# Kernel optimization log

Measured on AMD Instinct MI355X. Metric: run time of the kernel, lower is better.

The kernel has to match this reference:

```python
import jax, jax.numpy as jnp
import numpy as np

B, H, L, DIM = 4, 8, 1024, 256
D = DIM // H  # per-head dim
DEPTH, LAYER_I = 12, 1  # layer_index < depth//4 -> adjacency masking active


def _gcn(xh, adj, W):
    # One graph-convolution layer (GCN used as q/k/v projection in the repo):
    # support = x @ W per head, then aggregate with the (attention-)adjacency.
    # xh: [b,h,t,d], adj: [b,h,l,t], W: [d,d] -> [b,h,l,d]
    return jnp.einsum('bhlt,bhtd->bhld', adj, xh @ W)


def _split_heads(x):
    # 'b t (h d) -> b h t d'
    b, t, _ = x.shape
    return x.reshape(b, t, H, D).transpose(0, 2, 1, 3)


def _merge_heads(v):
    # 'b h t d -> b t (h d)'
    b, h, t, d = v.shape
    return v.transpose(0, 2, 1, 3).reshape(b, t, h * d)


def setup_inputs() -> dict:
    key = jax.random.key(0)
    ks = jax.random.split(key, 9)
    x = jax.random.normal(ks[0], (B, L, DIM), jnp.float32)
    resize_x = jax.random.normal(ks[1], (B, L, DIM), jnpp := jnp.float32) if False else jax.random.normal(ks[1], (B, L, DIM), jnp.float32)
    eye = jnp.eye(L, dtype=jnp.float32)[None, None]  # self-loops so no all-masked rows
    adj = jnp.clip((jax.random.uniform(ks[2], (B, H, L, L)) < 0.1).astype(jnp.float32) + eye, 0.0, 1.0)
    adj_resize = jnp.clip((jax.random.uniform(ks[3], (B, H, L, L)) < 0.1).astype(jnp.float32) + eye, 0.0, 1.0)
    s = D ** -0.5
    Wq = jax.random.normal(ks[4], (D, D), jnp.float32) * s
    Wk = jax.random.normal(ks[5], (D, D), jnp.float32) * s
    Wv = jax.random.normal(ks[6], (D, D), jnp.float32) * s
    R = jax.random.normal(ks[7], (H, H), jnp.float32)  # 'randomatrix' head-mixing param
    Wp = jax.random.normal(ks[8], (DIM, DIM), jnp.float32) * (DIM ** -0.5)  # proj_v (no bias)
    return {'x': x, 'resize_x': resize_x, 'adj': adj, 'adj_resize': adj_resize,
            'Wq': Wq, 'Wk': Wk, 'Wv': Wv, 'R': R, 'Wp': Wp}


def reference(x, resize_x, adj, adj_resize, Wq, Wk, Wv, R, Wp):
    scale = DIM ** -0.5  # note: torch code scales by dim**-0.5 (full dim, not d_head)
    xh = _split_heads(x)          # [b,h,l,d]
    rxh = _split_heads(resize_x)  # [b,h,t,d]
    q = _gcn(xh, adj, Wq)         # [b,h,l,d]
    k = _gcn(rxh, adj_resize, Wk)  # [b,h,t,d]
    attn = jnp.einsum('bhld,bhtd->bhlt', q, k) * scale
    attn = jax.nn.leaky_relu(attn, negative_slope=0.01)
    # cross-head mixing with learned HxH matrix: out[b,i] = sum_h R[i,h]*attn[b,h]
    attn = jnp.einsum('ih,bhlt->bilt', R, attn)
    if LAYER_I < DEPTH // 4:
        attn = jnp.where(adj > 0, attn, -jnp.inf)
    A = jax.nn.softmax(attn, axis=-1)                      # rep_adj
    Ar = jax.nn.softmax(A.transpose(0, 1, 3, 2), axis=-1)  # dual softmax on transpose
    v = _merge_heads(_gcn(xh, A, Wv))
    out = jax.nn.gelu(v, approximate=False) @ Wp
    vr = _merge_heads(_gcn(rxh, Ar, Wv))
    out_resize = jax.nn.gelu(vr, approximate=False) @ Wp
    return out, out_resize, A, Ar
```

## Files before the change

### kernel.cpp

```cpp
#include <hip/hip_runtime.h>
#include <hip/hip_bf16.h>
#include <math.h>

#define BB 4
#define HH 8
#define LL 1024
#define DD 32
#define DIMM 256

typedef unsigned short u16;
typedef short bf16x8 __attribute__((ext_vector_type(8)));
typedef float f32x4 __attribute__((ext_vector_type(4)));

__device__ __forceinline__ float bu2f(u16 s) {
  union { unsigned int u; float f; } cv; cv.u = ((unsigned int)s) << 16; return cv.f;
}
__device__ __forceinline__ u16 f2bu(float f) {
  union { float f; unsigned int u; } cv; cv.f = f;
  unsigned int u = cv.u;
  u += 0x7FFFu + ((u >> 16) & 1u);
  return (u16)(u >> 16);
}
__device__ __forceinline__ short f2bs(float f) {
  return (short)__bfloat16_as_ushort(__float2bfloat16(f));
}

__global__ __launch_bounds__(256) void k_proj(
    const float* __restrict__ x, const float* __restrict__ rx,
    const float* __restrict__ Wq, const float* __restrict__ Wk, const float* __restrict__ Wv,
    u16* __restrict__ xqT_hi, u16* __restrict__ xqT_lo,
    u16* __restrict__ xkT_hi, u16* __restrict__ xkT_lo,
    u16* __restrict__ xvT_hi, u16* __restrict__ xvrT_hi) {
  __shared__ float wq[32][32], wk[32][32], wv[32][32];
  __shared__ float xs[8][32], rxs[8][32];
  __shared__ float tq_[32][9], tk_[32][9], tv_[32][9], tvr_[32][9];
  int tid = threadIdx.x, bid = blockIdx.x;
  int chunk = bid & 127, h = (bid >> 7) & 7, b = bid >> 10;
  int t0 = chunk << 3;
  for (int i = tid; i < 1024; i += 256) {
    int r = i >> 5, c = i & 31;
    wq[r][c] = Wq[i]; wk[r][c] = Wk[i]; wv[r][c] = Wv[i];
  }
  int d = tid & 31, tl = tid >> 5;
  size_t xoff = ((size_t)b * LL + t0 + tl) * DIMM + h * 32 + d;
  xs[tl][d]  = x[xoff];
  rxs[tl][d] = rx[xoff];
  __syncthreads();
  float aq = 0.f, ak = 0.f, av = 0.f, ar = 0.f;
#pragma unroll
  for (int dp = 0; dp < 32; ++dp) {
    float xv_ = xs[tl][dp], rv_ = rxs[tl][dp];
    aq += xv_ * wq[dp][d];
    ak += rv_ * wk[dp][d];
    av += xv_ * wv[dp][d];
    ar += rv_ * wv[dp][d];
  }
  tq_[d][tl] = aq; tk_[d][tl] = ak; tv_[d][tl] = av; tvr_[d][tl] = ar;
  __syncthreads();
  int d2 = tid >> 3, t2 = tid & 7;
  size_t obase = ((size_t)((b * HH + h) * DD + d2)) * LL + t0 + t2;
  {
    float v = tq_[d2][t2]; u16 hi = f2bu(v);
    xqT_hi[obase] = hi; xqT_lo[obase] = f2bu(v - bu2f(hi));
  }
  {
    float v = tk_[d2][t2]; u16 hi = f2bu(v);
    xkT_hi[obase] = hi; xkT_lo[obase] = f2bu(v - bu2f(hi));
  }
  xvT_hi[obase]  = f2bu(tv_[d2][t2]);
  xvrT_hi[obase] = f2bu(tvr_[d2][t2]);
}

template<int PREC, int OUT_SPLIT>
__global__ __launch_bounds__(256) void k_wmat2(
    const float* __restrict__ wA, const float* __restrict__ wB,
    const u16* __restrict__ sAh, const u16* __restrict__ sAl,
    const u16* __restrict__ sBh, const u16* __restrict__ sBl,
    float* __restrict__ dA, float* __restrict__ dB,
    u16* __restrict__ dAhi, u16* __restrict__ dAlo,
    u16* __restrict__ dBhi, u16* __restrict__ dBlo) {
  int tid = threadIdx.x, bid = blockIdx.x;
  int sel = bid >> 9;
  const float* w  = sel ? wB : wA;
  const u16* sh   = sel ? sBh : sAh;
  const u16* sl   = sel ? sBl : sAl;
  float* dst      = sel ? dB : dA;
  u16* dhi        = sel ? dBhi : dAhi;
  u16* dlo        = sel ? dBlo : dAlo;
  int b2 = bid & 511;
  int lc = b2 & 15, bh = b2 >> 4;
  int wave = tid >> 6, lane = tid & 63;
  int l0 = (lc << 6) + (wave << 4);
  int col = lane & 15, g = lane >> 4;
  const float* wrow = w + ((size_t)bh * LL + l0 + col) * LL + (g << 3);
  const u16* b0h = sh + ((size_t)bh * DD + col) * LL + (g << 3);
  const u16* b1h = b0h + 16 * LL;
  const u16* b0l = PREC == 2 ? sl + ((size_t)bh * DD + col) * LL + (g << 3) : nullptr;
  const u16* b1l = PREC == 2 ? b0l + 16 * LL : nullptr;
  f32x4 acc0 = {0.f, 0.f, 0.f, 0.f}, acc1 = {0.f, 0.f, 0.f, 0.f};
#pragma unroll 2
  for (int t0 = 0; t0 < LL; t0 += 32) {
    f32x4 wa = *(const f32x4*)(wrow + t0);
    f32x4 wb = *(const f32x4*)(wrow + t0 + 4);
    bf16x8 whi;
#pragma unroll
    for (int i = 0; i < 4; ++i) {
      whi[i]     = f2bs(wa[i]);
      whi[i + 4] = f2bs(wb[i]);
    }
    bf16x8 s0h = *(const bf16x8*)(b0h + t0);
    bf16x8 s1h = *(const bf16x8*)(b1h + t0);
    acc0 = __builtin_amdgcn_mfma_f32_16x16x32_bf16(whi, s0h, acc0, 0, 0, 0);
    acc1 = __builtin_amdgcn_mfma_f32_16x16x32_bf16(whi, s1h, acc1, 0, 0, 0);
    if (PREC == 2) {
      bf16x8 s0l = *(const bf16x8*)(b0l + t0);
      bf16x8 s1l = *(const bf16x8*)(b1l + t0);
      acc0 = __builtin_amdgcn_mfma_f32_16x16x32_bf16(whi, s0l, acc0, 0, 0, 0);
      acc1 = __builtin_amdgcn_mfma_f32_16x16x32_bf16(whi, s1l, acc1, 0, 0, 0);
    }
  }
#pragma unroll
  for (int i = 0; i < 4; ++i) {
    size_t o = ((size_t)bh * LL + l0 + (g << 2) + i) * DD;
    if (OUT_SPLIT) {
      float v0 = acc0[i]; u16 h0 = f2bu(v0);
      dhi[o + col] = h0; dlo[o + col] = f2bu(v0 - bu2f(h0));
      float v1 = acc1[i]; u16 h1 = f2bu(v1);
      dhi[o + 16 + col] = h1; dlo[o + 16 + col] = f2bu(v1 - bu2f(h1));
    } else {
      dst[o + col] = acc0[i];
      dst[o + 16 + col] = acc1[i];
    }
  }
}

__global__ __launch_bounds__(256) void k_logits_mfma(
    const u16* __restrict__ qh, const u16* __restrict__ ql,
    const u16* __restrict__ kh, const u16* __restrict__ kl,
    const float* __restrict__ Rm, const float* __restrict__ adj,
    float* __restrict__ M) {
  __shared__ float Rlds[8][8];
  int tid = threadIdx.x, bid = blockIdx.x;
  int tb = bid & 7, lb = (bid >> 3) & 15, b = bid >> 7;
  int wave = tid >> 6, lane = tid & 63;
  int l0 = (lb << 6) + (wave << 4);
  int tbase = tb << 7;
  int idx16 = lane & 15, g = lane >> 4;
  if (tid < 64) Rlds[tid >> 3][tid & 7] = Rm[tid];
  bf16x8 qfh[8], qfl[8];
#pragma unroll
  for (int h = 0; h < 8; ++h) {
    size_t off = ((size_t)(b * HH + h) * LL + l0 + idx16) * DD + (g << 3);
    qfh[h] = *(const bf16x8*)(qh + off);
    qfl[h] = *(const bf16x8*)(ql + off);
  }
  __syncthreads();
  for (int tt = 0; tt < 8; ++tt) {
    int t = tbase + (tt << 4);
    f32x4 S[8];
#pragma unroll
    for (int h = 0; h < 8; ++h) {
      size_t koff = ((size_t)(b * HH + h) * LL + t + idx16) * DD + (g << 3);
      bf16x8 bh_ = *(const bf16x8*)(kh + koff);
      bf16x8 bl_ = *(const bf16x8*)(kl + koff);
      f32x4 s = {0.f, 0.f, 0.f, 0.f};
      s = __builtin_amdgcn_mfma_f32_16x16x32_bf16(qfh[h], bh_, s, 0, 0, 0);
      s = __builtin_amdgcn_mfma_f32_16x16x32_bf16(qfl[h], bh_, s, 0, 0, 0);
      s = __builtin_amdgcn_mfma_f32_16x16x32_bf16(qfh[h], bl_, s, 0, 0, 0);
      S[h] = s;
    }
#pragma unroll
    for (int h = 0; h < 8; ++h)
#pragma unroll
      for (int e = 0; e < 4; ++e) {
        float v = S[h][e] * 0.0625f;
        S[h][e] = (v > 0.f) ? v : 0.01f * v;
      }
    int lbase = l0 + (g << 2);
#pragma unroll
    for (int i = 0; i < 8; ++i) {
      float rr[8];
#pragma unroll
      for (int h = 0; h < 8; ++h) rr[h] = Rlds[i][h];
      size_t base = ((size_t)(b * HH + i) * LL + lbase) * LL + t + idx16;
#pragma unroll
      for (int e = 0; e < 4; ++e) {
        float m_ = 0.f;
#pragma unroll
        for (int h = 0; h < 8; ++h) m_ += rr[h] * S[h][e];
        float a = adj[base + (size_t)e * LL];
        M[base + (size_t)e * LL] = (a > 0.f) ? m_ : -INFINITY;
      }
    }
  }
}

__global__ __launch_bounds__(256) void k_norm2(
    float* __restrict__ A, float* __restrict__ colpart) {
  __shared__ float cacc[4][1024];
  int tid = threadIdx.x, bid = blockIdx.x;
  int ch = bid & 31, bh = bid >> 5;
  int wave = tid >> 6, lane = tid & 63;
  float4 colA[4];
#pragma unroll
  for (int j = 0; j < 4; ++j) colA[j] = make_float4(0.f, 0.f, 0.f, 0.f);
  for (int rr = 0; rr < 8; ++rr) {
    int l = (ch << 5) + (rr << 2) + wave;
    float4* Ap = (float4*)(A + ((size_t)bh * LL + l) * LL);
    float4 v[4];
#pragma unroll
    for (int j = 0; j < 4; ++j) v[j] = Ap[lane + (j << 6)];
    float mx = -INFINITY;
#pragma unroll
    for (int j = 0; j < 4; ++j)
      mx = fmaxf(mx, fmaxf(fmaxf(v[j].x, v[j].y), fmaxf(v[j].z, v[j].w)));
#pragma unroll
    for (int o = 32; o > 0; o >>= 1) mx = fmaxf(mx, __shfl_xor(mx, o, 64));
    float sm = 0.f;
#pragma unroll
    for (int j = 0; j < 4; ++j) {
      v[j].x = __expf(v[j].x - mx); v[j].y = __expf(v[j].y - mx);
      v[j].z = __expf(v[j].z - mx); v[j].w = __expf(v[j].w - mx);
      sm += v[j].x + v[j].y + v[j].z + v[j].w;
    }
#pragma unroll
    for (int o = 32; o > 0; o >>= 1) sm += __shfl_xor(sm, o, 64);
    float inv = 1.0f / sm;
#pragma unroll
    for (int j = 0; j < 4; ++j) {
      v[j].x *= inv; v[j].y *= inv; v[j].z *= inv; v[j].w *= inv;
      colA[j].x += __expf(v[j].x); colA[j].y += __expf(v[j].y);
      colA[j].z += __expf(v[j].z); colA[j].w += __expf(v[j].w);
      Ap[lane + (j << 6)] = v[j];
    }
  }
#pragma unroll
  for (int j = 0; j < 4; ++j)
    *(float4*)&cacc[wave][(j << 8) + (lane << 2)] = colA[j];
  __syncthreads();
  float4 s = make_float4(0.f, 0.f, 0.f, 0.f);
#pragma unroll
  for (int w = 0; w < 4; ++w) {
    float4 t = *(const float4*)&cacc[w][tid << 2];
    s.x += t.x; s.y += t.y; s.z += t.z; s.w += t.w;
  }
  ((float4*)(colpart + ((size_t)bh * 32 + ch) * LL))[tid] = s;
}

__global__ __launch_bounds__(256) void k_colred(
    const float* __restrict__ colpart, float* __restrict__ colsum) {
  int gid = blockIdx.x * 256 + threadIdx.x;
  int bh = gid >> 10, t = gid & 1023;
  const float* cp = colpart + (size_t)bh * 32 * LL + t;
  float s = 0.f;
#pragma unroll
  for (int c = 0; c < 32; ++c) s += cp[c * LL];
  colsum[gid] = s;
}

__global__ __launch_bounds__(256) void k_ar(
    const float* __restrict__ A, const float* __restrict__ colsum, float* __restrict__ Ar) {
  __shared__ float tile[64][65];
  int tid = threadIdx.x, bid = blockIdx.x;
  int tix = bid & 15, tiy = (bid >> 4) & 15, bh = bid >> 8;
  int l0 = tiy << 6, t0 = tix << 6;
  int c = tid & 63, r4 = tid >> 6;
  const float* Ab = A + ((size_t)bh * LL + l0) * LL + t0;
#pragma unroll
  for (int rr = 0; rr < 16; ++rr) {
    int li = (rr << 2) + r4;
    tile[li][c] = __expf(Ab[(size_t)li * LL + c]);
  }
  __syncthreads();
  float* Arb = Ar + ((size_t)bh * LL + t0) * LL + l0;
  const float* cs = colsum + bh * LL + t0;
#pragma unroll
  for (int rr = 0; rr < 16; ++rr) {
    int ti = (rr << 2) + r4;
    float inv = 1.0f / cs[ti];
    Arb[(size_t)ti * LL + c] = tile[c][ti] * inv;
  }
}

__global__ __launch_bounds__(256) void k_out2(
    const float* __restrict__ vb, const float* __restrict__ vrb,
    const float* __restrict__ Wp,
    float* __restrict__ out, float* __restrict__ outr) {
  __shared__ float g_s[16 * 256];
  __shared__ float wp_s[32 * 256];
  int tid = threadIdx.x, bid = blockIdx.x;
  int sel = bid >> 8;
  const float* vbuf = sel ? vrb : vb;
  float* o = sel ? outr : out;
  int b2 = bid & 255;
  int lt = b2 & 63, b = b2 >> 6;
  int l0 = lt << 4;
  int h = tid >> 5, dd = tid & 31;
#pragma unroll
  for (int r = 0; r < 16; ++r) {
    float v = vbuf[(((size_t)b * HH + h) * LL + l0 + r) * DD + dd];
    g_s[r * 256 + tid] = 0.5f * v * (1.0f + erff(v * 0.70710678118654752f));
  }
  float acc[16];
#pragma unroll
  for (int r = 0; r < 16; ++r) acc[r] = 0.f;
  for (int jc = 0; jc < 8; ++jc) {
    __syncthreads();
#pragma unroll
    for (int u = 0; u < 8; ++u) {
      int idx = tid + (u << 8);
      int j = idx >> 6, c4 = idx & 63;
      float4 v = *(const float4*)(Wp + (size_t)(jc * 32 + j) * DIMM + (c4 << 2));
      *(float4*)&wp_s[j * 256 + (c4 << 2)] = v;
    }
    __syncthreads();
#pragma unroll
    for (int j = 0; j < 32; ++j) {
      float wv = wp_s[j * 256 + tid];
      int jj = (jc << 5) + j;
#pragma unroll
      for (int r = 0; r < 16; ++r)
        acc[r] += g_s[r * 256 + jj] * wv;
    }
  }
#pragma unroll
  for (int r = 0; r < 16; ++r)
    o[((size_t)b * LL + l0 + r) * DIMM + tid] = acc[r];
}

extern "C" void kernel_launch(void* const* d_in, const int* in_sizes, int n_in,
                              void* d_out, int out_size, void* d_ws, size_t ws_size,
                              hipStream_t stream) {
  const float* x    = (const float*)d_in[0];
  const float* rx   = (const float*)d_in[1];
  const float* adj  = (const float*)d_in[2];
  const float* adjr = (const float*)d_in[3];
  const float* Wq   = (const float*)d_in[4];
  const float* Wk   = (const float*)d_in[5];
  const float* Wv   = (const float*)d_in[6];
  const float* Rm   = (const float*)d_in[7];
  const float* Wp   = (const float*)d_in[8];

  const size_t NE = (size_t)BB * HH * LL * DD;

  float* out  = (float*)d_out;
  float* outr = out + NE;
  float* A    = outr + NE;
  float* Ar   = A + (size_t)BB * HH * LL * LL;

  float* colpart = Ar;
  u16* q_hi   = (u16*)(Ar + NE);
  u16* q_lo   = q_hi + NE;
  u16* k_hi   = q_lo + NE;
  u16* k_lo   = k_hi + NE;
  u16* xqT_hi = k_lo + NE;
  u16* xqT_lo = xqT_hi + NE;
  u16* xkT_hi = xqT_lo + NE;
  u16* xkT_lo = xkT_hi + NE;
  u16* xvT_hi  = (u16*)out;
  u16* xvrT_hi = (u16*)outr;

  float* wsf    = (float*)d_ws;
  float* vb     = wsf;
  float* vrb    = wsf + NE;
  float* colsum = wsf + 2 * NE;

  k_proj<<<4096, 256, 0, stream>>>(x, rx, Wq, Wk, Wv,
                                   xqT_hi, xqT_lo, xkT_hi, xkT_lo,
                                   xvT_hi, xvrT_hi);
  k_wmat2<2,1><<<1024, 256, 0, stream>>>(adj, adjr,
                                         xqT_hi, xqT_lo, xkT_hi, xkT_lo,
                                         nullptr, nullptr,
                                         q_hi, q_lo, k_hi, k_lo);
  k_logits_mfma<<<512, 256, 0, stream>>>(q_hi, q_lo, k_hi, k_lo, Rm, adj, A);
  k_norm2<<<1024, 256, 0, stream>>>(A, colpart);
  k_colred<<<128, 256, 0, stream>>>(colpart, colsum);
  k_ar<<<8192, 256, 0, stream>>>(A, colsum, Ar);
  k_wmat2<1,0><<<1024, 256, 0, stream>>>(A, Ar,
                                         xvT_hi, nullptr, xvrT_hi, nullptr,
                                         vb, vrb,
                                         nullptr, nullptr, nullptr, nullptr);
  k_out2<<<512, 256, 0, stream>>>(vb, vrb, Wp, out, outr);
}
```

Before: 453.1 us.

## Pack adjacency mask into bits during q GCN and coalesce logits stores

While the first GCN kernel streams the fp32 adjacency, it also writes a packed bitmask (one bit per entry). The logits kernel then reads that bitmask instead of re-reading the full 128 MB fp32 adjacency. It also transposes each 16x16 result tile through LDS so the masked logits are written as float4 row-contiguous stores instead of scattered scalar ones. The costs are an extra byte store per iteration in the GCN kernel, the LDS round-trip in the logits kernel, and some workspace for the bits.

```diff
diff --git a/kernel.cpp b/kernel.cpp
--- a/kernel.cpp
+++ b/kernel.cpp
@@ -9,6 +9,7 @@
 #define DIMM 256
 
 typedef unsigned short u16;
+typedef unsigned int u32;
 typedef short bf16x8 __attribute__((ext_vector_type(8)));
 typedef float f32x4 __attribute__((ext_vector_type(4)));
 
@@ -71,14 +72,15 @@
   xvrT_hi[obase] = f2bu(tvr_[d2][t2]);
 }
 
-template<int PREC, int OUT_SPLIT>
+template<int PREC, int OUT_SPLIT, int WRITE_BITS>
 __global__ __launch_bounds__(256) void k_wmat2(
     const float* __restrict__ wA, const float* __restrict__ wB,
     const u16* __restrict__ sAh, const u16* __restrict__ sAl,
     const u16* __restrict__ sBh, const u16* __restrict__ sBl,
     float* __restrict__ dA, float* __restrict__ dB,
     u16* __restrict__ dAhi, u16* __restrict__ dAlo,
-    u16* __restrict__ dBhi, u16* __restrict__ dBlo) {
+    u16* __restrict__ dBhi, u16* __restrict__ dBlo,
+    u32* __restrict__ bits) {
   int tid = threadIdx.x, bid = blockIdx.x;
   int sel = bid >> 9;
   const float* w  = sel ? wB : wA;
@@ -97,6 +99,9 @@
   const u16* b1h = b0h + 16 * LL;
   const u16* b0l = PREC == 2 ? sl + ((size_t)bh * DD + col) * LL + (g << 3) : nullptr;
   const u16* b1l = PREC == 2 ? b0l + 16 * LL : nullptr;
+  unsigned char* bytep = nullptr;
+  if (WRITE_BITS && sel == 0)
+    bytep = (unsigned char*)(bits + (size_t)bh * 32 * LL + l0 + col) + g;
   f32x4 acc0 = {0.f, 0.f, 0.f, 0.f}, acc1 = {0.f, 0.f, 0.f, 0.f};
 #pragma unroll 2
   for (int t0 = 0; t0 < LL; t0 += 32) {
@@ -107,6 +112,15 @@
     for (int i = 0; i < 4; ++i) {
       whi[i]     = f2bs(wa[i]);
       whi[i + 4] = f2bs(wb[i]);
+    }
+    if (WRITE_BITS && sel == 0) {
+      unsigned int byte = 0;
+#pragma unroll
+      for (int i = 0; i < 4; ++i) {
+        byte |= (wa[i] > 0.f ? 1u : 0u) << i;
+        byte |= (wb[i] > 0.f ? 1u : 0u) << (4 + i);
+      }
+      bytep[(size_t)(t0 >> 5) * (LL * 4)] = (unsigned char)byte;
     }
     bf16x8 s0h = *(const bf16x8*)(b0h + t0);
     bf16x8 s1h = *(const bf16x8*)(b1h + t0);
@@ -137,9 +151,10 @@
 __global__ __launch_bounds__(256) void k_logits_mfma(
     const u16* __restrict__ qh, const u16* __restrict__ ql,
     const u16* __restrict__ kh, const u16* __restrict__ kl,
-    const float* __restrict__ Rm, const float* __restrict__ adj,
+    const float* __restrict__ Rm, const u32* __restrict__ bits,
     float* __restrict__ M) {
   __shared__ float Rlds[8][8];
+  __shared__ float mtile[4][16 * 17];
   int tid = threadIdx.x, bid = blockIdx.x;
   int tb = bid & 7, lb = (bid >> 3) & 15, b = bid >> 7;
   int wave = tid >> 6, lane = tid & 63;
@@ -155,6 +170,7 @@
     qfl[h] = *(const bf16x8*)(ql + off);
   }
   __syncthreads();
+  int rr_ = lane >> 2, c0 = (lane & 3) << 2;
   for (int tt = 0; tt < 8; ++tt) {
     int t = tbase + (tt << 4);
     f32x4 S[8];
@@ -176,21 +192,33 @@
         float v = S[h][e] * 0.0625f;
         S[h][e] = (v > 0.f) ? v : 0.01f * v;
       }
-    int lbase = l0 + (g << 2);
+    int word = t >> 5;
+    int bitpos = ((tt & 1) << 4) + idx16;
 #pragma unroll
     for (int i = 0; i < 8; ++i) {
-      float rr[8];
-#pragma unroll
-      for (int h = 0; h < 8; ++h) rr[h] = Rlds[i][h];
-      size_t base = ((size_t)(b * HH + i) * LL + lbase) * LL + t + idx16;
+      float rr8[8];
+#pragma unroll
+      for (int h = 0; h < 8; ++h) rr8[h] = Rlds[i][h];
+      const u32* bp = bits + ((size_t)(b * HH + i) * 32 + word) * LL + l0 + (g << 2);
+      u32 mw0 = bp[0], mw1 = bp[1], mw2 = bp[2], mw3 = bp[3];
+      float m_[4];
 #pragma unroll
       for (int e = 0; e < 4; ++e) {
-        float m_ = 0.f;
-#pragma unroll
-        for (int h = 0; h < 8; ++h) m_ += rr[h] * S[h][e];
-        float a = adj[base + (size_t)e * LL];
-        M[base + (size_t)e * LL] = (a > 0.f) ? m_ : -INFINITY;
+        float acc = 0.f;
+#pragma unroll
+        for (int h = 0; h < 8; ++h) acc += rr8[h] * S[h][e];
+        u32 mw = (e == 0) ? mw0 : (e == 1) ? mw1 : (e == 2) ? mw2 : mw3;
+        m_[e] = ((mw >> bitpos) & 1u) ? acc : -INFINITY;
       }
+#pragma unroll
+      for (int e = 0; e < 4; ++e)
+        mtile[wave][((g << 2) + e) * 17 + idx16] = m_[e];
+      float4 v4;
+      v4.x = mtile[wave][rr_ * 17 + c0 + 0];
+      v4.y = mtile[wave][rr_ * 17 + c0 + 1];
+      v4.z = mtile[wave][rr_ * 17 + c0 + 2];
+      v4.w = mtile[wave][rr_ * 17 + c0 + 3];
+      *(float4*)(M + ((size_t)(b * HH + i) * LL + l0 + rr_) * LL + t + c0) = v4;
     }
   }
 }
@@ -364,21 +392,22 @@
   float* vb     = wsf;
   float* vrb    = wsf + NE;
   float* colsum = wsf + 2 * NE;
+  u32* adjbits  = (u32*)(wsf + 2 * NE + 32768);
 
   k_proj<<<4096, 256, 0, stream>>>(x, rx, Wq, Wk, Wv,
                                    xqT_hi, xqT_lo, xkT_hi, xkT_lo,
                                    xvT_hi, xvrT_hi);
-  k_wmat2<2,1><<<1024, 256, 0, stream>>>(adj, adjr,
-                                         xqT_hi, xqT_lo, xkT_hi, xkT_lo,
-                                         nullptr, nullptr,
-                                         q_hi, q_lo, k_hi, k_lo);
-  k_logits_mfma<<<512, 256, 0, stream>>>(q_hi, q_lo, k_hi, k_lo, Rm, adj, A);
+  k_wmat2<2,1,1><<<1024, 256, 0, stream>>>(adj, adjr,
+                                           xqT_hi, xqT_lo, xkT_hi, xkT_lo,
+                                           nullptr, nullptr,
+                                           q_hi, q_lo, k_hi, k_lo, adjbits);
+  k_logits_mfma<<<512, 256, 0, stream>>>(q_hi, q_lo, k_hi, k_lo, Rm, adjbits, A);
   k_norm2<<<1024, 256, 0, stream>>>(A, colpart);
   k_colred<<<128, 256, 0, stream>>>(colpart, colsum);
   k_ar<<<8192, 256, 0, stream>>>(A, colsum, Ar);
-  k_wmat2<1,0><<<1024, 256, 0, stream>>>(A, Ar,
-                                         xvT_hi, nullptr, xvrT_hi, nullptr,
-                                         vb, vrb,
-                                         nullptr, nullptr, nullptr, nullptr);
+  k_wmat2<1,0,0><<<1024, 256, 0, stream>>>(A, Ar,
+                                           xvT_hi, nullptr, xvrT_hi, nullptr,
+                                           vb, vrb,
+                                           nullptr, nullptr, nullptr, nullptr, nullptr);
   k_out2<<<512, 256, 0, stream>>>(vb, vrb, Wp, out, outr);
 }
```

Measured after the change: 423.4 us. 1.07x faster.
